# Performance work log

Measured on AMD Instinct MI355X. Metric: run time of the kernel, lower is better.

Reference implementation:

```python
import jax, jax.numpy as jnp
import numpy as np

B, C, CE, H, W = 4, 128, 64, 64, 64
V = H * W
# parent(i) < i//2 guarantees depth <= ceil(log2(V)) = 12; 14 is a safe static bound
MAX_LEVELS = 14


def _gather_v(x, idx):
    # x: [B, C, V], idx: [B, V] -> gather along vertex dim (broadcast over C)
    return jnp.take_along_axis(x, idx[:, None, :], axis=2)


def _tree_filter(feature_in, embed_in, sorted_index, sorted_parent, node_level):
    Bv, Cv, Hv, Wv = feature_in.shape
    Vv = Hv * Wv
    f = feature_in.reshape(Bv, Cv, Vv)
    e = embed_in.reshape(Bv, embed_in.shape[1], Vv)
    # build_edge_weight: gather to BFS order, gather parent, squared-L2 distance, exp(-d)
    f_s = _gather_v(f, sorted_index)          # [B,C,V] features in topological order
    e_s = _gather_v(e, sorted_index)
    e_p = _gather_v(e_s, sorted_parent)
    d2 = jnp.sum((e_s - e_p) ** 2, axis=1)    # [B,V]
    w = jnp.exp(-d2)                          # edge weight node->parent (root: exp(0)=1, unused)
    wB = w[:, None, :]
    # ---- up sweep (leaves -> root), level-parallel over BFS levels ----
    # A_i = f_i + sum_{c in child(i)} w_c * A_c ; Z_i = 1 + sum w_c * Z_c (self_weight = 1)
    aggr_up = f_s
    nrm_up = jnp.ones((Bv, Vv), feature_in.dtype)
    for d in range(MAX_LEVELS - 1, 0, -1):
        mw = jnp.where(node_level == d, w, jnp.zeros((), feature_in.dtype))
        aggr_up = jax.vmap(lambda a, p, m: a.at[:, p].add(m))(
            aggr_up, sorted_parent, mw[:, None, :] * aggr_up)
        nrm_up = jax.vmap(lambda a, p, m: a.at[p].add(m))(
            nrm_up, sorted_parent, mw * nrm_up)
    # ---- down sweep (root -> leaves) ----
    # Ahat_i = A_i + w_i * (Ahat_parent - w_i * A_i); root keeps A_root
    aggr = aggr_up
    nrm = nrm_up
    for d in range(1, MAX_LEVELS):
        sel = node_level == d
        pa = _gather_v(aggr, sorted_parent)
        aggr = jnp.where(sel[:, None, :], aggr_up + wB * (pa - wB * aggr_up), aggr)
        pn = jnp.take_along_axis(nrm, sorted_parent, axis=1)
        nrm = jnp.where(sel, nrm_up + w * (pn - w * nrm_up), nrm)
    out_s = aggr / nrm[:, None, :]
    # scatter back from BFS order to original vertex order
    out = jax.vmap(lambda o, i: jnp.zeros_like(o).at[:, i].set(o))(out_s, sorted_index)
    return out.reshape(Bv, Cv, Hv, Wv)


def setup_inputs() -> dict:
    key = jax.random.key(0)
    k1, k2 = jax.random.split(key)
    feature_in = jax.random.normal(k1, (B, C, H, W), dtype=jnp.float32)
    embed_in = 0.1 * jax.random.normal(k2, (B, CE, H, W), dtype=jnp.float32)
    rng = np.random.default_rng(0)
    sorted_index = np.stack([rng.permutation(V) for _ in range(B)]).astype(np.int32)
    sorted_parent = np.zeros((B, V), dtype=np.int32)
    node_level = np.zeros((B, V), dtype=np.int32)
    for b in range(B):
        for i in range(1, V):
            p = int(rng.integers(0, max(1, i // 2)))  # parent earlier in order, depth <= log2(V)
            sorted_parent[b, i] = p
            node_level[b, i] = node_level[b, p] + 1
    return {
        "feature_in": feature_in,
        "embed_in": embed_in,
        "sorted_index": jnp.asarray(sorted_index),
        "sorted_parent": jnp.asarray(sorted_parent),
        "node_level": jnp.asarray(node_level),
    }


def reference(feature_in, embed_in, sorted_index, sorted_parent, node_level):
    return _tree_filter(feature_in, embed_in, sorted_index, sorted_parent, node_level)
```

## Files before the change

kernel.cpp:

```cpp
#include <hip/hip_runtime.h>

#define BB 4
#define CC 128
#define CE 64
#define VV 4096
#define NLEV 14


__device__ __forceinline__ void lds_fadd(float* p, float v) {
    unsafeAtomicAdd(p, v);
}

__global__ __launch_bounds__(256) void prep_kernel(
    const float* __restrict__ embed,
    const int* __restrict__ sorted_index,
    const int* __restrict__ sorted_parent,
    const int* __restrict__ node_level,
    float* __restrict__ wsort,
    int*   __restrict__ giInv,
    int2*  __restrict__ cpl,
    int*   __restrict__ offs)
{
    int tid = threadIdx.x;
    if (blockIdx.x < BB) {
        int b = blockIdx.x;
        __shared__ int si_s[VV];
        __shared__ int pos_s[VV];
        __shared__ int lo_s[VV];
        __shared__ int hist[NLEV + 1];
        __shared__ int cursor[NLEV];
        __shared__ int offSh[NLEV + 1];
        const int* lev = node_level    + b * VV;
        const int* si  = sorted_index  + b * VV;
        const int* par = sorted_parent + b * VV;

        if (tid < NLEV + 1) hist[tid] = 0;
        __syncthreads();
        for (int i = tid; i < VV; i += 256) {
            si_s[i] = si[i];
            int d = lev[i]; d = d < NLEV - 1 ? d : NLEV - 1;
            atomicAdd(&hist[d], 1);
        }
        __syncthreads();
        if (tid == 0) {
            int acc = 0;
            for (int d = 0; d < NLEV; ++d) { int h = hist[d]; offSh[d] = acc; cursor[d] = acc; acc += h; }
            offSh[NLEV] = acc;
        }
        __syncthreads();
        if (tid <= NLEV) offs[b * 16 + tid] = offSh[tid];
        for (int i = tid; i < VV; i += 256) {
            int d = lev[i]; d = d < NLEV - 1 ? d : NLEV - 1;
            int k = atomicAdd(&cursor[d], 1);
            pos_s[i] = k;
            lo_s[k]  = i;
            giInv[b * VV + si_s[i]] = k;
        }
        __syncthreads();
        for (int k = tid; k < VV; k += 256) {
            int i = lo_s[k];
            cpl[b * VV + k] = make_int2(pos_s[par[i]], i);
        }
    } else {
        __shared__ float part[4][64];
        int bb   = blockIdx.x - BB;
        int b    = bb >> 6;
        int n0   = (bb & 63) << 6;
        int lane = tid & 63;
        int w    = tid >> 6;
        int i    = n0 + lane;
        int vi = sorted_index[b * VV + i];
        int p  = sorted_parent[b * VV + i];
        int vp = sorted_index[b * VV + p];
        const float* eb = embed + (size_t)b * CE * VV;
        float acc = 0.f;
        #pragma unroll
        for (int r = 0; r < 16; ++r) {
            int ce = w * 16 + r;
            float d = eb[ce * VV + vi] - eb[ce * VV + vp];
            acc = fmaf(d, d, acc);
        }
        part[w][lane] = acc;
        __syncthreads();
        if (w == 0) {
            float d2 = part[0][lane] + part[1][lane] + part[2][lane] + part[3][lane];
            wsort[b * VV + i] = __expf(-d2);
        }
    }
}

__global__ __launch_bounds__(256) void tree_kernel(
    const float* __restrict__ feat,
    const float* __restrict__ wsort,
    const int*  __restrict__ giInv,
    const int2* __restrict__ cpl,
    const int*  __restrict__ offs,
    float* __restrict__ out)
{
    __shared__ float2 vv[VV];
    __shared__ int    cw[VV];
    __shared__ int    offS[16];
    int b   = blockIdx.x >> 7;
    int c   = blockIdx.x & (CC - 1);
    int tid = threadIdx.x;

    const int2*  cplB = cpl   + b * VV;
    const int*   ivB  = giInv + b * VV;
    const float* wsB  = wsort + b * VV;
    const float* f    = feat + ((size_t)(b * CC + c)) * VV;

    if (tid < 16) offS[tid] = offs[b * 16 + tid];

    #pragma unroll
    for (int t = 0; t < 16; ++t) {
        int k = tid + t * 256;
        int2 x = cplB[k];
        int wb = __float_as_int(wsB[x.y]);
        cw[k] = (wb & 0xFFFFF000) | x.x;
    }

    int4 kkR[4];
    #pragma unroll
    for (int t = 0; t < 4; ++t) {
        int idx = tid + t * 256;
        float4 fv = ((const float4*)f)[idx];
        int4   kk = ((const int4*)ivB)[idx];
        kkR[t] = kk;
        vv[kk.x] = make_float2(fv.x, 1.f);
        vv[kk.y] = make_float2(fv.y, 1.f);
        vv[kk.z] = make_float2(fv.z, 1.f);
        vv[kk.w] = make_float2(fv.w, 1.f);
    }
    __syncthreads();

    for (int d = NLEV - 1; d >= 1; --d) {
        int s = offS[d], e = offS[d + 1];
        if (s == e) continue;
        for (int k = s + tid; k < e; k += 256) {
            int x = cw[k];
            float w = __int_as_float(x & 0xFFFFF000);
            int  cp = x & 0xFFF;
            float2 u = vv[k];
            lds_fadd(&vv[cp].x, w * u.x);
            lds_fadd(&vv[cp].y, w * u.y);
        }
        __syncthreads();
    }

    for (int d = 1; d <= NLEV - 1; ++d) {
        int s = offS[d], e = offS[d + 1];
        if (s == e) continue;
        for (int k = s + tid; k < e; k += 256) {
            int x = cw[k];
            float w = __int_as_float(x & 0xFFFFF000);
            int  cp = x & 0xFFF;
            float2 u  = vv[k];
            float2 pa = vv[cp];
            vv[k] = make_float2(fmaf(w, fmaf(-w, u.x, pa.x), u.x),
                                fmaf(w, fmaf(-w, u.y, pa.y), u.y));
        }
        __syncthreads();
    }

    float* ob = out + ((size_t)(b * CC + c)) * VV;
    #pragma unroll
    for (int t = 0; t < 4; ++t) {
        int idx = tid + t * 256;
        int4 kk = kkR[t];
        float2 u0 = vv[kk.x];
        float2 u1 = vv[kk.y];
        float2 u2 = vv[kk.z];
        float2 u3 = vv[kk.w];
        float4 r;
        r.x = __fdividef(u0.x, u0.y);
        r.y = __fdividef(u1.x, u1.y);
        r.z = __fdividef(u2.x, u2.y);
        r.w = __fdividef(u3.x, u3.y);
        ((float4*)ob)[idx] = r;
    }
}

extern "C" void kernel_launch(void* const* d_in, const int* in_sizes, int n_in,
                              void* d_out, int out_size, void* d_ws, size_t ws_size,
                              hipStream_t stream) {
    const float* feat          = (const float*)d_in[0];
    const float* embed         = (const float*)d_in[1];
    const int*   sorted_index  = (const int*)d_in[2];
    const int*   sorted_parent = (const int*)d_in[3];
    const int*   node_level    = (const int*)d_in[4];
    float* out = (float*)d_out;

    char* ws = (char*)d_ws;
    const size_t A = (size_t)BB * VV * 4;
    float* wsort = (float*)(ws);
    int*   giInv = (int*)  (ws + A);
    int2*  cpl   = (int2*) (ws + 2 * A);
    int*   offs  = (int*)  (ws + 4 * A);

    prep_kernel<<<BB + BB * 64, 256, 0, stream>>>(
        embed, sorted_index, sorted_parent, node_level, wsort, giInv, cpl, offs);

    tree_kernel<<<BB * CC, 256, 0, stream>>>(
        feat, wsort, giInv, cpl, offs, out);
}
```

Baseline: 116.8 us.

## Fuse prep and tree kernels into one cooperative launch with grid sync

Merges the preprocessing kernel (level sort and edge weights) and the per-channel tree filter kernel into a single cooperative kernel separated by a grid-wide barrier. Edge-weight computation is spread over the remaining blocks with four lanes per node and shuffle reductions instead of the old shared-memory partials. Shared memory is aliased between the two phases. This removes one kernel launch and its inter-kernel gap, but adds a grid sync and requires all 512 blocks to be co-resident.

```diff
diff --git a/kernel.cpp b/kernel.cpp
--- a/kernel.cpp
+++ b/kernel.cpp
@@ -1,35 +1,46 @@
 #include <hip/hip_runtime.h>
+#include <hip/hip_cooperative_groups.h>
+
+namespace cg = cooperative_groups;
 
 #define BB 4
 #define CC 128
 #define CE 64
 #define VV 4096
 #define NLEV 14
+#define NNODE (BB * VV)
+#define GRID  (BB * CC)
+#define WBLK  (GRID - BB)
+#define NPB   33
 
 
 __device__ __forceinline__ void lds_fadd(float* p, float v) {
     unsafeAtomicAdd(p, v);
 }
 
-__global__ __launch_bounds__(256) void prep_kernel(
+__global__ __launch_bounds__(256) void fused_kernel(
+    const float* __restrict__ feat,
     const float* __restrict__ embed,
-    const int* __restrict__ sorted_index,
-    const int* __restrict__ sorted_parent,
-    const int* __restrict__ node_level,
+    const int*  __restrict__ sorted_index,
+    const int*  __restrict__ sorted_parent,
+    const int*  __restrict__ node_level,
     float* __restrict__ wsort,
     int*   __restrict__ giInv,
     int2*  __restrict__ cpl,
-    int*   __restrict__ offs)
+    int*   __restrict__ offs,
+    float* __restrict__ out)
 {
+    __shared__ __align__(16) int lds[3 * VV];
+    __shared__ int hist[NLEV + 1];
+    __shared__ int cursor[NLEV];
+    __shared__ int offSh[NLEV + 1];
     int tid = threadIdx.x;
+
     if (blockIdx.x < BB) {
         int b = blockIdx.x;
-        __shared__ int si_s[VV];
-        __shared__ int pos_s[VV];
-        __shared__ int lo_s[VV];
-        __shared__ int hist[NLEV + 1];
-        __shared__ int cursor[NLEV];
-        __shared__ int offSh[NLEV + 1];
+        int* si_s  = lds;
+        int* pos_s = lds + VV;
+        int* lo_s  = lds + 2 * VV;
         const int* lev = node_level    + b * VV;
         const int* si  = sorted_index  + b * VV;
         const int* par = sorted_parent + b * VV;
@@ -62,47 +73,38 @@
             cpl[b * VV + k] = make_int2(pos_s[par[i]], i);
         }
     } else {
-        __shared__ float part[4][64];
-        int bb   = blockIdx.x - BB;
-        int b    = bb >> 6;
-        int n0   = (bb & 63) << 6;
-        int lane = tid & 63;
-        int w    = tid >> 6;
-        int i    = n0 + lane;
-        int vi = sorted_index[b * VV + i];
-        int p  = sorted_parent[b * VV + i];
-        int vp = sorted_index[b * VV + p];
-        const float* eb = embed + (size_t)b * CE * VV;
-        float acc = 0.f;
-        #pragma unroll
-        for (int r = 0; r < 16; ++r) {
-            int ce = w * 16 + r;
-            float d = eb[ce * VV + vi] - eb[ce * VV + vp];
-            acc = fmaf(d, d, acc);
-        }
-        part[w][lane] = acc;
-        __syncthreads();
-        if (w == 0) {
-            float d2 = part[0][lane] + part[1][lane] + part[2][lane] + part[3][lane];
-            wsort[b * VV + i] = __expf(-d2);
-        }
-    }
-}
-
-__global__ __launch_bounds__(256) void tree_kernel(
-    const float* __restrict__ feat,
-    const float* __restrict__ wsort,
-    const int*  __restrict__ giInv,
-    const int2* __restrict__ cpl,
-    const int*  __restrict__ offs,
-    float* __restrict__ out)
-{
-    __shared__ float2 vv[VV];
-    __shared__ int    cw[VV];
-    __shared__ int    offS[16];
-    int b   = blockIdx.x >> 7;
-    int c   = blockIdx.x & (CC - 1);
-    int tid = threadIdx.x;
+        int base = (blockIdx.x - BB) * NPB;
+        int nl   = tid >> 2;
+        int ch   = tid & 3;
+        int g    = base + nl;
+        if (nl < NPB && g < NNODE) {
+            int b = g >> 12;
+            int i = g & (VV - 1);
+            int vi = sorted_index[g];
+            int p  = sorted_parent[g];
+            int vp = sorted_index[b * VV + p];
+            const float* eb = embed + (size_t)b * CE * VV;
+            float acc = 0.f;
+            #pragma unroll
+            for (int r = 0; r < 16; ++r) {
+                int ce = ch * 16 + r;
+                float d = eb[ce * VV + vi] - eb[ce * VV + vp];
+                acc = fmaf(d, d, acc);
+            }
+            acc += __shfl_xor(acc, 1, 64);
+            acc += __shfl_xor(acc, 2, 64);
+            if (ch == 0) wsort[g] = __expf(-acc);
+        }
+    }
+
+    __threadfence();
+    cg::this_grid().sync();
+
+    float2* vv = (float2*)lds;
+    int*    cw = lds + 2 * VV;
+    __shared__ int offS[16];
+    int b = blockIdx.x >> 7;
+    int c = blockIdx.x & (CC - 1);
 
     const int2*  cplB = cpl   + b * VV;
     const int*   ivB  = giInv + b * VV;
@@ -197,9 +199,11 @@
     int2*  cpl   = (int2*) (ws + 2 * A);
     int*   offs  = (int*)  (ws + 4 * A);
 
-    prep_kernel<<<BB + BB * 64, 256, 0, stream>>>(
-        embed, sorted_index, sorted_parent, node_level, wsort, giInv, cpl, offs);
-
-    tree_kernel<<<BB * CC, 256, 0, stream>>>(
-        feat, wsort, giInv, cpl, offs, out);
+    void* args[] = {
+        (void*)&feat, (void*)&embed, (void*)&sorted_index, (void*)&sorted_parent,
+        (void*)&node_level, (void*)&wsort, (void*)&giInv, (void*)&cpl,
+        (void*)&offs, (void*)&out
+    };
+    hipLaunchCooperativeKernel((const void*)fused_kernel,
+                               dim3(GRID), dim3(256), args, 0, stream);
 }
```

After: 243.0 us. +108.0%, slower.

## Process two channels per block to share normalizer and edge-weight setup

Applied to the files above, without the earlier changes.

Each tree block now handles two feature channels with 512 threads, keeping separate LDS arrays for both channels plus one shared normalizer array. The normalizer sweep and the packed edge-weight/parent table build are done once per channel pair instead of once per channel, which cuts LDS atomics and setup loads. In exchange the grid halves to 256 blocks, so fewer blocks are available to spread across CUs, and LDS per block grows to about 64KB, which may limit occupancy.

```diff
diff --git a/kernel.cpp b/kernel.cpp
--- a/kernel.cpp
+++ b/kernel.cpp
@@ -89,7 +89,7 @@
     }
 }
 
-__global__ __launch_bounds__(256) void tree_kernel(
+__global__ __launch_bounds__(512) void tree2_kernel(
     const float* __restrict__ feat,
     const float* __restrict__ wsort,
     const int*  __restrict__ giInv,
@@ -97,52 +97,55 @@
     const int*  __restrict__ offs,
     float* __restrict__ out)
 {
-    __shared__ float2 vv[VV];
-    __shared__ int    cw[VV];
-    __shared__ int    offS[16];
-    int b   = blockIdx.x >> 7;
-    int c   = blockIdx.x & (CC - 1);
+    __shared__ float val0[VV];
+    __shared__ float val1[VV];
+    __shared__ float nrm[VV];
+    __shared__ int   cw[VV];
+    __shared__ int   offS[16];
+    int b   = blockIdx.x >> 6;
+    int c0  = (blockIdx.x & 63) << 1;
     int tid = threadIdx.x;
 
     const int2*  cplB = cpl   + b * VV;
     const int*   ivB  = giInv + b * VV;
     const float* wsB  = wsort + b * VV;
-    const float* f    = feat + ((size_t)(b * CC + c)) * VV;
+    const float* f0   = feat + ((size_t)(b * CC + c0)) * VV;
+    const float* f1   = f0 + VV;
 
     if (tid < 16) offS[tid] = offs[b * 16 + tid];
 
     #pragma unroll
-    for (int t = 0; t < 16; ++t) {
-        int k = tid + t * 256;
+    for (int t = 0; t < 8; ++t) {
+        int k = tid + t * 512;
         int2 x = cplB[k];
         int wb = __float_as_int(wsB[x.y]);
         cw[k] = (wb & 0xFFFFF000) | x.x;
     }
 
-    int4 kkR[4];
+    int4 kkR[2];
     #pragma unroll
-    for (int t = 0; t < 4; ++t) {
-        int idx = tid + t * 256;
-        float4 fv = ((const float4*)f)[idx];
+    for (int t = 0; t < 2; ++t) {
+        int idx = tid + t * 512;
         int4   kk = ((const int4*)ivB)[idx];
+        float4 a  = ((const float4*)f0)[idx];
+        float4 bq = ((const float4*)f1)[idx];
         kkR[t] = kk;
-        vv[kk.x] = make_float2(fv.x, 1.f);
-        vv[kk.y] = make_float2(fv.y, 1.f);
-        vv[kk.z] = make_float2(fv.z, 1.f);
-        vv[kk.w] = make_float2(fv.w, 1.f);
+        val0[kk.x] = a.x;  val0[kk.y] = a.y;  val0[kk.z] = a.z;  val0[kk.w] = a.w;
+        val1[kk.x] = bq.x; val1[kk.y] = bq.y; val1[kk.z] = bq.z; val1[kk.w] = bq.w;
+        nrm[kk.x] = 1.f;   nrm[kk.y] = 1.f;   nrm[kk.z] = 1.f;   nrm[kk.w] = 1.f;
     }
     __syncthreads();
 
     for (int d = NLEV - 1; d >= 1; --d) {
         int s = offS[d], e = offS[d + 1];
         if (s == e) continue;
-        for (int k = s + tid; k < e; k += 256) {
+        for (int k = s + tid; k < e; k += 512) {
             int x = cw[k];
             float w = __int_as_float(x & 0xFFFFF000);
             int  cp = x & 0xFFF;
-            float2 u = vv[k];
-            lds_fadd(&vv[cp].x, w * u.x);
-            lds_fadd(&vv[cp].y, w * u.y);
+            lds_fadd(&val0[cp], w * val0[k]);
+            lds_fadd(&val1[cp], w * val1[k]);
+            lds_fadd(&nrm[cp],  w * nrm[k]);
         }
         __syncthreads();
     }
@@ -150,33 +153,35 @@
     for (int d = 1; d <= NLEV - 1; ++d) {
         int s = offS[d], e = offS[d + 1];
         if (s == e) continue;
-        for (int k = s + tid; k < e; k += 256) {
+        for (int k = s + tid; k < e; k += 512) {
             int x = cw[k];
             float w = __int_as_float(x & 0xFFFFF000);
             int  cp = x & 0xFFF;
-            float2 u  = vv[k];
-            float2 pa = vv[cp];
-            vv[k] = make_float2(fmaf(w, fmaf(-w, u.x, pa.x), u.x),
-                                fmaf(w, fmaf(-w, u.y, pa.y), u.y));
-        }
-        __syncthreads();
-    }
-
-    float* ob = out + ((size_t)(b * CC + c)) * VV;
+            float u0 = val0[k], u1 = val1[k], un = nrm[k];
+            val0[k] = fmaf(w, fmaf(-w, u0, val0[cp]), u0);
+            val1[k] = fmaf(w, fmaf(-w, u1, val1[cp]), u1);
+            nrm[k]  = fmaf(w, fmaf(-w, un, nrm[cp]),  un);
+        }
+        __syncthreads();
+    }
+
+    float* o0 = out + ((size_t)(b * CC + c0)) * VV;
+    float* o1 = o0 + VV;
     #pragma unroll
-    for (int t = 0; t < 4; ++t) {
-        int idx = tid + t * 256;
+    for (int t = 0; t < 2; ++t) {
+        int idx = tid + t * 512;
         int4 kk = kkR[t];
-        float2 u0 = vv[kk.x];
-        float2 u1 = vv[kk.y];
-        float2 u2 = vv[kk.z];
-        float2 u3 = vv[kk.w];
-        float4 r;
-        r.x = __fdividef(u0.x, u0.y);
-        r.y = __fdividef(u1.x, u1.y);
-        r.z = __fdividef(u2.x, u2.y);
-        r.w = __fdividef(u3.x, u3.y);
-        ((float4*)ob)[idx] = r;
+        float i0 = __fdividef(1.f, nrm[kk.x]);
+        float i1 = __fdividef(1.f, nrm[kk.y]);
+        float i2 = __fdividef(1.f, nrm[kk.z]);
+        float i3 = __fdividef(1.f, nrm[kk.w]);
+        float4 r0, r1;
+        r0.x = val0[kk.x] * i0; r0.y = val0[kk.y] * i1;
+        r0.z = val0[kk.z] * i2; r0.w = val0[kk.w] * i3;
+        r1.x = val1[kk.x] * i0; r1.y = val1[kk.y] * i1;
+        r1.z = val1[kk.z] * i2; r1.w = val1[kk.w] * i3;
+        ((float4*)o0)[idx] = r0;
+        ((float4*)o1)[idx] = r1;
     }
 }
 
@@ -200,6 +205,6 @@
     prep_kernel<<<BB + BB * 64, 256, 0, stream>>>(
         embed, sorted_index, sorted_parent, node_level, wsort, giInv, cpl, offs);
 
-    tree_kernel<<<BB * CC, 256, 0, stream>>>(
+    tree2_kernel<<<BB * CC / 2, 512, 0, stream>>>(
         feat, wsort, giInv, cpl, offs, out);
 }
```

Result: faster. 110.3 us (-5.6%).
